# Optimization experiments

Measured on AMD Instinct MI355X. Metric: run time of the kernel, lower is better.

Reference implementation:

```python
import jax, jax.numpy as jnp
import numpy as np

BN_EPS = 1e-5
INTERP_EPS = 1e-8


def setup_inputs() -> dict:
    key = jax.random.key(0)
    ks = jax.random.split(key, 8)
    B, N, S, D1, D2 = 8, 8192, 2048, 128, 256
    C_in, C_mid, C_out = D1 + D2, 256, 256
    return {
        "xyz1": jax.random.normal(ks[0], (B, 3, N), dtype=jnp.float32),
        "xyz2": jax.random.normal(ks[1], (B, 3, S), dtype=jnp.float32),
        "points1": jax.random.normal(ks[2], (B, D1, N), dtype=jnp.float32),
        "points2": jax.random.normal(ks[3], (B, D2, S), dtype=jnp.float32),
        "W0": jax.random.normal(ks[4], (C_mid, C_in), dtype=jnp.float32) * (1.0 / np.sqrt(C_in)),
        "b0": jnp.zeros((C_mid,), dtype=jnp.float32),
        "gamma0": jnp.ones((C_mid,), dtype=jnp.float32),
        "beta0": jnp.zeros((C_mid,), dtype=jnp.float32),
        "W1": jax.random.normal(ks[5], (C_out, C_mid), dtype=jnp.float32) * (1.0 / np.sqrt(C_mid)),
        "b1": jnp.zeros((C_out,), dtype=jnp.float32),
    }


def reference(xyz1, xyz2, points1, points2, W0, b0, gamma0, beta0, W1, b1):
    B, _, N = xyz1.shape
    S = xyz2.shape[2]
    x1 = jnp.transpose(xyz1, (0, 2, 1))  # (B, N, 3)
    x2 = jnpp = jnp.transpose(xyz2, (0, 2, 1))  # (B, S, 3)
    # squared distances: (B, N, S)
    d = (jnp.sum(x1 ** 2, -1)[:, :, None]
         + jnp.sum(x2 ** 2, -1)[:, None, :]
         - 2.0 * jnp.einsum('bnc,bsc->bns', x1, x2))
    # 3 nearest neighbors (fused top-3 instead of full sort; same math)
    neg_d, idx = jax.lax.top_k(-d, 3)  # (B, N, 3)
    dists = -neg_d
    recip = 1.0 / (dists + INTERP_EPS)
    weight = recip / jnp.sum(recip, axis=2, keepdims=True)  # (B, N, 3)
    p2t = jnp.transpose(points2, (0, 2, 1))  # (B, S, D2)
    D2 = p2t.shape[-1]
    gathered = jnp.take_along_axis(p2t, idx.reshape(B, N * 3, 1), axis=1).reshape(B, N, 3, D2)
    interp = jnp.einsum('bnkc,bnk->bcn', gathered, weight)  # (B, D2, N)
    new_points = jnp.concatenate([interp, points1], axis=1)  # (B, D2+D1, N)
    # conv0 (1x1) + BatchNorm (train mode, batch stats) + ReLU
    h = jnp.einsum('oc,bcn->bon', W0, new_points) + b0[None, :, None]
    mean = jnp.mean(h, axis=(0, 2), keepdims=True)
    var = jnp.mean((h - mean) ** 2, axis=(0, 2), keepdims=True)  # biased, as torch BN
    h = gamma0[None, :, None] * (h - mean) * jax.lax.rsqrt(var + BN_EPS) + beta0[None, :, None]
    h = jax.nn.relu(h)
    # conv1 (1x1) + Identity (module pairs conv1 with nn.Identity) + ReLU
    h = jnp.einsum('oc,bcn->bon', W1, h) + b1[None, :, None]
    return jax.nn.relu(h)
```

## Files before the change

kernel.cpp:

```cpp
#include <hip/hip_runtime.h>
#include <stdint.h>

constexpr int B = 8, N = 8192, S = 2048, D1 = 128, D2 = 256;
constexpr int CIN = 384, CMID = 256, COUT = 256;

typedef __attribute__((ext_vector_type(8))) _Float16 half8;
typedef __attribute__((ext_vector_type(4))) _Float16 half4;
typedef __attribute__((ext_vector_type(4))) float f32x4;

union HU { uint32_t u; _Float16 h[2]; };


__global__ __launch_bounds__(256) void k_top3(const float* __restrict__ xyz1,
                                              const float* __restrict__ xyz2,
                                              uint32_t* __restrict__ pw3) {
  __shared__ float4 Pq[S];
  __shared__ float md[4][3][128];
  __shared__ int mi[4][3][128];
  __shared__ float snrm[128];
  const int tid = threadIdx.x;
  const int wv = tid >> 6, lane = tid & 63;
  const int b = blockIdx.y;
  const int nb = blockIdx.x * 128;
  const float* x1 = xyz1 + (size_t)b * 3 * N;
  const float* x2 = xyz2 + (size_t)b * 3 * S;

  for (int j = tid; j < S; j += 256) {
    float sx = x2[j], sy = x2[j + S], sz = x2[j + 2 * S];
    Pq[j] = float4{sx, sy, sz, sx * sx + sy * sy + sz * sz};
  }
  float nax[2], nay[2], naz[2];
#pragma unroll
  for (int t = 0; t < 2; ++t) {
    const int n = nb + t * 64 + lane;
    const float ax = x1[n], ay = x1[n + N], az = x1[n + 2 * N];
    nax[t] = -2.f * ax; nay[t] = -2.f * ay; naz[t] = -2.f * az;
    if (wv == 0) snrm[t * 64 + lane] = ax * ax + ay * ay + az * az;
  }
  __syncthreads();

  float e0[2], e1[2], e2[2];
  int j0[2], j1[2], j2[2];
#pragma unroll
  for (int t = 0; t < 2; ++t) {
    e0[t] = 1e30f; e1[t] = 1e30f; e2[t] = 1e30f;
    j0[t] = 0; j1[t] = 0; j2[t] = 0;
  }
  const int s0 = wv * (S / 4), s1 = s0 + (S / 4);
#pragma unroll 4
  for (int s = s0; s < s1; ++s) {
    const float4 v = Pq[s];
#pragma unroll
    for (int t = 0; t < 2; ++t) {
      const float d = fmaf(nax[t], v.x, fmaf(nay[t], v.y, fmaf(naz[t], v.z, v.w)));
      const bool c0 = d < e0[t], c1 = d < e1[t], c2 = d < e2[t];
      const int u2 = c1 ? j1[t] : s;
      const int u1 = c0 ? j0[t] : s;
      j2[t] = c2 ? u2 : j2[t];
      j1[t] = c1 ? u1 : j1[t];
      j0[t] = c0 ? s : j0[t];
      e2[t] = __builtin_amdgcn_fmed3f(e1[t], e2[t], d);
      e1[t] = __builtin_amdgcn_fmed3f(e0[t], e1[t], d);
      e0[t] = fminf(e0[t], d);
    }
  }
#pragma unroll
  for (int t = 0; t < 2; ++t) {
    const int idx = t * 64 + lane;
    md[wv][0][idx] = e0[t]; mi[wv][0][idx] = j0[t];
    md[wv][1][idx] = e1[t]; mi[wv][1][idx] = j1[t];
    md[wv][2][idx] = e2[t]; mi[wv][2][idx] = j2[t];
  }
  __syncthreads();
  if (tid < 128) {
    float f0 = md[0][0][tid], f1 = md[0][1][tid], f2 = md[0][2][tid];
    int g0 = mi[0][0][tid], g1 = mi[0][1][tid], g2 = mi[0][2][tid];
#pragma unroll
    for (int w = 1; w < 4; ++w)
#pragma unroll
      for (int k = 0; k < 3; ++k) {
        float d = md[w][k][tid];
        int i = mi[w][k][tid];
        if (d < f2) {
          if (d < f1) {
            f2 = f1; g2 = g1;
            if (d < f0) { f1 = f0; g1 = g0; f0 = d; g0 = i; }
            else        { f1 = d;  g1 = i; }
          } else { f2 = d; g2 = i; }
        }
      }
    const float rn = snrm[tid];
    float q0 = fmaxf(f0 + rn, 0.f);
    float q1 = fmaxf(f1 + rn, 0.f);
    float q2 = fmaxf(f2 + rn, 0.f);
    float r0 = 1.0f / (q0 + 1e-8f), r1 = 1.0f / (q1 + 1e-8f), r2 = 1.0f / (q2 + 1e-8f);
    float inv = 1.0f / (r0 + r1 + r2);
    auto pack = [](int i, float w) -> uint32_t {
      uint32_t q = (uint32_t)(w * 2097152.0f + 0.5f);
      if (q > 0x1FFFFFu) q = 0x1FFFFFu;
      return ((uint32_t)i << 21) | q;
    };
    size_t base = ((size_t)b * N + nb + tid) * 3;
    pw3[base]     = pack(g0, r0 * inv);
    pw3[base + 1] = pack(g1, r1 * inv);
    pw3[base + 2] = pack(g2, r2 * inv);
  }
}

__global__ __launch_bounds__(256) void k_G(const float* __restrict__ points2,
                                           const float* __restrict__ W0,
                                           float* __restrict__ dout) {
  __shared__ half8 A_lds[4][256];
  __shared__ half8 B_lds[4][32];
  __shared__ float CT[32][258];
  const int tid = threadIdx.x;
  const int b = blockIdx.x >> 6;
  const int s0 = (blockIdx.x & 63) * 32;
  f32x4 acc[4][2] = {};
  const int wv = tid >> 6, lane = tid & 63;
  const int ln = lane & 15, quad = lane >> 4;
  const int bn = tid & 31, bkc = tid >> 5;
  const int ar = tid >> 3, ac4 = tid & 7;

  for (int kk = 0; kk < 256; kk += 32) {
    __syncthreads();
#pragma unroll
    for (int p = 0; p < 8; ++p) {
      int row = ar + 32 * p;
      const float4 v = *(const float4*)(W0 + (size_t)row * CIN + kk + ac4 * 4);
      half4 hv = {(_Float16)v.x, (_Float16)v.y, (_Float16)v.z, (_Float16)v.w};
      *(half4*)((_Float16*)&A_lds[ac4 >> 1][row] + (ac4 & 1) * 4) = hv;
    }
    {
      half4 hv;
#pragma unroll
      for (int j = 0; j < 4; ++j)
        hv[j] = (_Float16)points2[((size_t)(b * 256 + kk + bkc * 4 + j)) * S + s0 + bn];
      *(half4*)((_Float16*)&B_lds[bkc >> 1][bn] + (bkc & 1) * 4) = hv;
    }
    __syncthreads();
    half8 af[4], bf[2];
#pragma unroll
    for (int i = 0; i < 4; ++i) af[i] = A_lds[quad][wv * 64 + i * 16 + ln];
#pragma unroll
    for (int j = 0; j < 2; ++j) bf[j] = B_lds[quad][j * 16 + ln];
#pragma unroll
    for (int i = 0; i < 4; ++i)
#pragma unroll
      for (int j = 0; j < 2; ++j)
        acc[i][j] = __builtin_amdgcn_mfma_f32_16x16x32_f16(af[i], bf[j], acc[i][j], 0, 0, 0);
  }
  __syncthreads();
#pragma unroll
  for (int i = 0; i < 4; ++i)
#pragma unroll
    for (int reg = 0; reg < 4; ++reg) {
      int row = wv * 64 + i * 16 + quad * 4 + reg;
#pragma unroll
      for (int j = 0; j < 2; ++j) CT[j * 16 + ln][row] = acc[i][j][reg];
    }
  __syncthreads();
  const int sl = tid >> 3, g = tid & 7;
  float* g0 = dout + ((size_t)(b * 256 + 128)) * 8192 + (size_t)(s0 + sl) * 256 + g * 32;
#pragma unroll
  for (int q = 0; q < 8; ++q)
    *(float4*)(g0 + q * 4) = *(const float4*)&CT[sl][g * 32 + q * 4];
}

__global__ __launch_bounds__(256) void k_interp(const uint32_t* __restrict__ pw3,
                                                const float* __restrict__ dout_c,
                                                uint32_t* __restrict__ dout_u) {
  __shared__ int sidx[96];
  __shared__ float sw[96];
  const int tid = threadIdx.x;
  const int b = blockIdx.x >> 8;
  const int n0 = (blockIdx.x & 255) * 32;
  if (tid < 96) {
    uint32_t p = pw3[((size_t)b * N + n0) * 3 + tid];
    sidx[tid] = (int)(p >> 21);
    sw[tid] = (float)(p & 0x1FFFFFu) * (1.0f / 2097152.0f);
  }
  __syncthreads();
  const int colL = tid >> 3, p = tid & 7;
  const float* Gb = dout_c + ((size_t)(b * 256 + 128)) * 8192;
  float a[32];
#pragma unroll
  for (int q = 0; q < 32; ++q) a[q] = 0.f;
#pragma unroll
  for (int k = 0; k < 3; ++k) {
    int j = sidx[colL * 3 + k];
    float w = sw[colL * 3 + k];
    const float* g = Gb + (size_t)j * 256 + p * 32;
#pragma unroll
    for (int q = 0; q < 8; ++q) {
      float4 v = *(const float4*)(g + q * 4);
      a[q * 4 + 0] += w * v.x; a[q * 4 + 1] += w * v.y;
      a[q * 4 + 2] += w * v.z; a[q * 4 + 3] += w * v.w;
    }
  }
#pragma unroll
  for (int q = 0; q < 16; ++q) {
    int cp = p * 16 + q;
    HU u;
    u.h[0] = (_Float16)a[2 * q];
    u.h[1] = (_Float16)a[2 * q + 1];
    dout_u[((size_t)(b * 256 + cp)) * 8192 + n0 + colL] = u.u;
  }
}

__global__ __launch_bounds__(256) void k_w1h(const float* __restrict__ W1,
                                             _Float16* __restrict__ W1h) {
  const int gid = blockIdx.x * 256 + threadIdx.x;
  const float4 v = *(const float4*)(W1 + (size_t)gid * 4);
  half4 h = {(_Float16)v.x, (_Float16)v.y, (_Float16)v.z, (_Float16)v.w};
  *(half4*)(W1h + (size_t)gid * 4) = h;
}

__global__ __launch_bounds__(256) void k_h(uint32_t* __restrict__ h2,
                                           float* __restrict__ dpart,
                                           const float* __restrict__ points1,
                                           const float* __restrict__ W0,
                                           const float* __restrict__ b0) {
  __shared__ half8 A_lds[4][256];
  __shared__ half8 B_lds[4][64];
  __shared__ float red_s[256], red_q[256], sb0[256];
  const int tid = threadIdx.x;
  const int b = blockIdx.x >> 7;
  const int cb = blockIdx.x & 127;
  const int n0 = cb * 64;
  sb0[tid] = b0[tid];
  f32x4 acc[4][4] = {};
  const int wv = tid >> 6, lane = tid & 63;
  const int ln = lane & 15, quad = lane >> 4;
  const int bn = tid & 63, bkc = tid >> 6;
  const int ar = tid >> 3, ac4 = tid & 7;

  for (int kk = 0; kk < 128; kk += 32) {
    __syncthreads();
#pragma unroll
    for (int p = 0; p < 8; ++p) {
      int row = ar + 32 * p;
      const float4 v = *(const float4*)(W0 + (size_t)row * CIN + 256 + kk + ac4 * 4);
      half4 hv = {(_Float16)v.x, (_Float16)v.y, (_Float16)v.z, (_Float16)v.w};
      *(half4*)((_Float16*)&A_lds[ac4 >> 1][row] + (ac4 & 1) * 4) = hv;
    }
    {
      half8 hv;
#pragma unroll
      for (int j = 0; j < 8; ++j)
        hv[j] = (_Float16)points1[((size_t)(b * D1 + kk + bkc * 8 + j)) * N + n0 + bn];
      B_lds[bkc][bn] = hv;
    }
    __syncthreads();
    half8 af[4], bf[4];
#pragma unroll
    for (int i = 0; i < 4; ++i) af[i] = A_lds[quad][wv * 64 + i * 16 + ln];
#pragma unroll
    for (int j = 0; j < 4; ++j) bf[j] = B_lds[quad][j * 16 + ln];
#pragma unroll
    for (int i = 0; i < 4; ++i)
#pragma unroll
      for (int j = 0; j < 4; ++j)
        acc[i][j] = __builtin_amdgcn_mfma_f32_16x16x32_f16(af[i], bf[j], acc[i][j], 0, 0, 0);
  }
#pragma unroll
  for (int i = 0; i < 4; ++i) {
    const int rb = wv * 64 + i * 16 + quad * 4;
    const int cp0 = rb >> 1;
    float rs[4] = {0.f, 0.f, 0.f, 0.f}, rq[4] = {0.f, 0.f, 0.f, 0.f};
#pragma unroll
    for (int jj = 0; jj < 4; ++jj) {
      const int col = n0 + jj * 16 + ln;
      size_t a0 = ((size_t)(b * 256 + cp0)) * 8192 + col;
      HU ua, ub;
      ua.u = h2[a0];
      ub.u = h2[a0 + 8192];
      _Float16 e0 = (_Float16)(acc[i][jj][0] + (float)ua.h[0] + sb0[rb + 0]);
      _Float16 e1 = (_Float16)(acc[i][jj][1] + (float)ua.h[1] + sb0[rb + 1]);
      _Float16 e2 = (_Float16)(acc[i][jj][2] + (float)ub.h[0] + sb0[rb + 2]);
      _Float16 e3 = (_Float16)(acc[i][jj][3] + (float)ub.h[1] + sb0[rb + 3]);
      HU o0, o1;
      o0.h[0] = e0; o0.h[1] = e1; o1.h[0] = e2; o1.h[1] = e3;
      h2[a0] = o0.u;
      h2[a0 + 8192] = o1.u;
      float f0 = (float)e0, f1 = (float)e1, f2 = (float)e2, f3 = (float)e3;
      rs[0] += f0; rq[0] += f0 * f0;
      rs[1] += f1; rq[1] += f1 * f1;
      rs[2] += f2; rq[2] += f2 * f2;
      rs[3] += f3; rq[3] += f3 * f3;
    }
#pragma unroll
    for (int reg = 0; reg < 4; ++reg) {
      float s = rs[reg], q = rq[reg];
#pragma unroll
      for (int m = 1; m < 16; m <<= 1) {
        s += __shfl_xor(s, m);
        q += __shfl_xor(q, m);
      }
      if (ln == 0) { red_s[rb + reg] = s; red_q[rb + reg] = q; }
    }
  }
  __syncthreads();
  float* part = dpart + ((size_t)(b * 256 + 192)) * 8192 + (size_t)cb * 512;
  part[tid] = red_s[tid];
  part[256 + tid] = red_q[tid];
}

__global__ __launch_bounds__(256) void k_bn(const float* __restrict__ dpart,
                                            const float* __restrict__ gamma,
                                            const float* __restrict__ beta,
                                            float* __restrict__ bna,
                                            float* __restrict__ bnb) {
  const int c = blockIdx.x;
  const int tid = threadIdx.x;
  float s = 0.f, q = 0.f;
#pragma unroll
  for (int u = tid; u < 1024; u += 256) {
    int b = u >> 7, cb = u & 127;
    const float* part = dpart + ((size_t)(b * 256 + 192)) * 8192 + (size_t)cb * 512;
    s += part[c];
    q += part[256 + c];
  }
#pragma unroll
  for (int m = 1; m < 64; m <<= 1) {
    s += __shfl_xor(s, m);
    q += __shfl_xor(q, m);
  }
  __shared__ float ls[4], lq[4];
  if ((tid & 63) == 0) { ls[tid >> 6] = s; lq[tid >> 6] = q; }
  __syncthreads();
  if (tid == 0) {
    float st = ls[0] + ls[1] + ls[2] + ls[3];
    float qt = lq[0] + lq[1] + lq[2] + lq[3];
    const float invn = 1.0f / (float)(B * N);
    float mean = st * invn;
    float var = qt * invn - mean * mean;
    float a = gamma[c] * rsqrtf(var + 1e-5f);
    bna[c] = a;
    bnb[c] = beta[c] - mean * a;
  }
}

__global__ __launch_bounds__(256) void k_fused1(const uint32_t* h2,
                                                const _Float16* __restrict__ W1h,
                                                const float* __restrict__ b1,
                                                const float* __restrict__ bna,
                                                const float* __restrict__ bnb,
                                                float* out) {
  __shared__ uint32_t Hh[32 * 33 * 4];
  __shared__ float sa[256], sb[256], sb1[256];
  const int tid = threadIdx.x;
  const int b = blockIdx.x >> 8;
  const int n0 = (blockIdx.x & 255) * 32;
  sa[tid] = bna[tid]; sb[tid] = bnb[tid]; sb1[tid] = b1[tid];
  __syncthreads();
  {
    const int c4 = tid & 7;
    const int rg = tid >> 3;
#pragma unroll
    for (int q = 0; q < 4; ++q) {
      const int cp = rg + 32 * q;
      const uint4 v = *(const uint4*)&h2[((size_t)(b * 256 + cp)) * 8192 + n0 + c4 * 4];
      const int k0 = 2 * cp;
      const float a0 = sa[k0], a1 = sa[k0 + 1], b0v = sb[k0], b1v = sb[k0 + 1];
      const int kc = cp >> 2, sub = cp & 3;
      const uint32_t vv[4] = {v.x, v.y, v.z, v.w};
#pragma unroll
      for (int m = 0; m < 4; ++m) {
        HU u; u.u = vv[m];
        float v0 = a0 * (float)u.h[0] + b0v;
        float v1 = a1 * (float)u.h[1] + b1v;
        HU o;
        o.h[0] = (_Float16)(v0 > 0.f ? v0 : 0.f);
        o.h[1] = (_Float16)(v1 > 0.f ? v1 : 0.f);
        Hh[((kc * 33) + c4 * 4 + m) * 4 + sub] = o.u;
      }
    }
  }
  __syncthreads();
  f32x4 acc[4][2] = {};
  const int wv = tid >> 6, lane = tid & 63;
  const int ln = lane & 15, quad = lane >> 4;
  for (int kk = 0; kk < 256; kk += 32) {
    half8 af[4], bf[2];
#pragma unroll
    for (int i = 0; i < 4; ++i) {
      int row = wv * 64 + i * 16 + ln;
      af[i] = *(const half8*)(W1h + (size_t)row * CMID + kk + quad * 8);
    }
#pragma unroll
    for (int j = 0; j < 2; ++j)
      bf[j] = *(const half8*)&Hh[(((kk >> 3) + quad) * 33 + j * 16 + ln) * 4];
#pragma unroll
    for (int i = 0; i < 4; ++i)
#pragma unroll
      for (int j = 0; j < 2; ++j)
        acc[i][j] = __builtin_amdgcn_mfma_f32_16x16x32_f16(af[i], bf[j], acc[i][j], 0, 0, 0);
  }
#pragma unroll
  for (int i = 0; i < 4; ++i) {
    const int rb = wv * 64 + i * 16 + quad * 4;
#pragma unroll
    for (int reg = 0; reg < 4; ++reg) {
      int row = rb + reg;
      float bias = sb1[row];
      float* orow = out + ((size_t)(b * 256 + row)) * 8192 + n0;
#pragma unroll
      for (int j = 0; j < 2; ++j)
        orow[j * 16 + ln] = fmaxf(acc[i][j][reg] + bias, 0.f);
    }
  }
}

extern "C" void kernel_launch(void* const* d_in, const int* in_sizes, int n_in,
                              void* d_out, int out_size, void* d_ws, size_t ws_size,
                              hipStream_t stream) {
  const float* xyz1 = (const float*)d_in[0];
  const float* xyz2 = (const float*)d_in[1];
  const float* points1 = (const float*)d_in[2];
  const float* points2 = (const float*)d_in[3];
  const float* W0 = (const float*)d_in[4];
  const float* b0 = (const float*)d_in[5];
  const float* gamma0 = (const float*)d_in[6];
  const float* beta0 = (const float*)d_in[7];
  const float* W1 = (const float*)d_in[8];
  const float* b1 = (const float*)d_in[9];
  float* out = (float*)d_out;

  char* ws = (char*)d_ws;
  float* bna = (float*)ws;
  float* bnb = (float*)(ws + 1024);
  uint32_t* pw3 = (uint32_t*)(ws + 2048);
  _Float16* W1h = (_Float16*)(ws + 2048);

  k_top3<<<dim3(N / 128, B), 256, 0, stream>>>(xyz1, xyz2, pw3);
  k_G<<<dim3(B * 64), 256, 0, stream>>>(points2, W0, out);
  k_interp<<<dim3(B * N / 32), 256, 0, stream>>>(pw3, out, (uint32_t*)out);
  k_w1h<<<dim3(64), 256, 0, stream>>>(W1, W1h);
  k_h<<<dim3(B * N / 64), 256, 0, stream>>>((uint32_t*)out, out, points1, W0, b0);
  k_bn<<<dim3(256), 256, 0, stream>>>(out, gamma0, beta0, bna, bnb);
  k_fused1<<<dim3(B * N / 32), 256, 0, stream>>>((const uint32_t*)out, W1h, b1,
                                                 bna, bnb, out);
}
```

Measured before the change: 319.2 us.

## Prepack W0 tail to fp16 and stream A fragments directly in k_h

The fp32-to-fp16 conversion of W0's points1 columns moves into a combined weight-pack kernel, so k_h reads half8 A fragments straight from global memory instead of converting and staging them through LDS every k-step. k_h now uses 32-column tiles (twice as many blocks), loads all of points1 into LDS once with a single barrier, and preloads the interp partial result into the accumulators. It also removes the per-iteration barriers. The cost is more blocks, more BN partials to reduce in k_bn, and repeated global reads of W0h that rely on cache hits.

```diff
diff --git a/kernel.cpp b/kernel.cpp
--- a/kernel.cpp
+++ b/kernel.cpp
@@ -208,59 +208,86 @@
   }
 }
 
-__global__ __launch_bounds__(256) void k_w1h(const float* __restrict__ W1,
-                                             _Float16* __restrict__ W1h) {
-  const int gid = blockIdx.x * 256 + threadIdx.x;
-  const float4 v = *(const float4*)(W1 + (size_t)gid * 4);
-  half4 h = {(_Float16)v.x, (_Float16)v.y, (_Float16)v.z, (_Float16)v.w};
-  *(half4*)(W1h + (size_t)gid * 4) = h;
+__global__ __launch_bounds__(256) void k_wpack(const float* __restrict__ W0,
+                                               const float* __restrict__ W1,
+                                               _Float16* __restrict__ W1h,
+                                               _Float16* __restrict__ W0h) {
+  const int bid = blockIdx.x;
+  if (bid < 64) {
+    const int gid = bid * 256 + threadIdx.x;
+    const float4 v = *(const float4*)(W1 + (size_t)gid * 4);
+    half4 h = {(_Float16)v.x, (_Float16)v.y, (_Float16)v.z, (_Float16)v.w};
+    *(half4*)(W1h + (size_t)gid * 4) = h;
+  } else {
+    const int gid = (bid - 64) * 256 + threadIdx.x;
+    const int row = gid >> 5, c4 = gid & 31;
+    const float4 v = *(const float4*)(W0 + (size_t)row * CIN + 256 + c4 * 4);
+    half4 h = {(_Float16)v.x, (_Float16)v.y, (_Float16)v.z, (_Float16)v.w};
+    *(half4*)(W0h + (size_t)row * 128 + c4 * 4) = h;
+  }
 }
 
 __global__ __launch_bounds__(256) void k_h(uint32_t* __restrict__ h2,
                                            float* __restrict__ dpart,
                                            const float* __restrict__ points1,
-                                           const float* __restrict__ W0,
+                                           const _Float16* __restrict__ W0h,
                                            const float* __restrict__ b0) {
-  __shared__ half8 A_lds[4][256];
-  __shared__ half8 B_lds[4][64];
+  __shared__ half8 B_lds[16][32];
   __shared__ float red_s[256], red_q[256], sb0[256];
   const int tid = threadIdx.x;
-  const int b = blockIdx.x >> 7;
-  const int cb = blockIdx.x & 127;
-  const int n0 = cb * 64;
+  const int b = blockIdx.x >> 8;
+  const int cb = blockIdx.x & 255;
+  const int n0 = cb * 32;
   sb0[tid] = b0[tid];
-  f32x4 acc[4][4] = {};
   const int wv = tid >> 6, lane = tid & 63;
   const int ln = lane & 15, quad = lane >> 4;
-  const int bn = tid & 63, bkc = tid >> 6;
-  const int ar = tid >> 3, ac4 = tid & 7;
-
+
+  f32x4 acc[4][2];
+#pragma unroll
+  for (int i = 0; i < 4; ++i) {
+    const int rb = wv * 64 + i * 16 + quad * 4;
+    const int cp0 = rb >> 1;
+#pragma unroll
+    for (int j = 0; j < 2; ++j) {
+      const int col = n0 + j * 16 + ln;
+      const size_t a0 = ((size_t)(b * 256 + cp0)) * 8192 + col;
+      HU ua, ub;
+      ua.u = h2[a0];
+      ub.u = h2[a0 + 8192];
+      acc[i][j][0] = (float)ua.h[0];
+      acc[i][j][1] = (float)ua.h[1];
+      acc[i][j][2] = (float)ub.h[0];
+      acc[i][j][3] = (float)ub.h[1];
+    }
+  }
+  {
+    const int col = tid & 31;
+    const int kc0 = tid >> 5;
+#pragma unroll
+    for (int it = 0; it < 2; ++it) {
+      const int kc = kc0 + 8 * it;
+      half8 hv;
+#pragma unroll
+      for (int j = 0; j < 8; ++j)
+        hv[j] = (_Float16)points1[((size_t)(b * D1 + kc * 8 + j)) * N + n0 + col];
+      B_lds[kc][col] = hv;
+    }
+  }
+  __syncthreads();
   for (int kk = 0; kk < 128; kk += 32) {
-    __syncthreads();
-#pragma unroll
-    for (int p = 0; p < 8; ++p) {
-      int row = ar + 32 * p;
-      const float4 v = *(const float4*)(W0 + (size_t)row * CIN + 256 + kk + ac4 * 4);
-      half4 hv = {(_Float16)v.x, (_Float16)v.y, (_Float16)v.z, (_Float16)v.w};
-      *(half4*)((_Float16*)&A_lds[ac4 >> 1][row] + (ac4 & 1) * 4) = hv;
-    }
-    {
-      half8 hv;
-#pragma unroll
-      for (int j = 0; j < 8; ++j)
-        hv[j] = (_Float16)points1[((size_t)(b * D1 + kk + bkc * 8 + j)) * N + n0 + bn];
-      B_lds[bkc][bn] = hv;
-    }
-    __syncthreads();
-    half8 af[4], bf[4];
-#pragma unroll
-    for (int i = 0; i < 4; ++i) af[i] = A_lds[quad][wv * 64 + i * 16 + ln];
-#pragma unroll
-    for (int j = 0; j < 4; ++j) bf[j] = B_lds[quad][j * 16 + ln];
+    half8 af[4], bf[2];
+#pragma unroll
+    for (int i = 0; i < 4; ++i) {
+      const int row = wv * 64 + i * 16 + ln;
+      af[i] = *(const half8*)(W0h + (size_t)row * 128 + kk + quad * 8);
+    }
+#pragma unroll
+    for (int j = 0; j < 2; ++j)
+      bf[j] = B_lds[(kk >> 3) + quad][j * 16 + ln];
 #pragma unroll
     for (int i = 0; i < 4; ++i)
 #pragma unroll
-      for (int j = 0; j < 4; ++j)
+      for (int j = 0; j < 2; ++j)
         acc[i][j] = __builtin_amdgcn_mfma_f32_16x16x32_f16(af[i], bf[j], acc[i][j], 0, 0, 0);
   }
 #pragma unroll
@@ -269,16 +296,13 @@
     const int cp0 = rb >> 1;
     float rs[4] = {0.f, 0.f, 0.f, 0.f}, rq[4] = {0.f, 0.f, 0.f, 0.f};
 #pragma unroll
-    for (int jj = 0; jj < 4; ++jj) {
-      const int col = n0 + jj * 16 + ln;
-      size_t a0 = ((size_t)(b * 256 + cp0)) * 8192 + col;
-      HU ua, ub;
-      ua.u = h2[a0];
-      ub.u = h2[a0 + 8192];
-      _Float16 e0 = (_Float16)(acc[i][jj][0] + (float)ua.h[0] + sb0[rb + 0]);
-      _Float16 e1 = (_Float16)(acc[i][jj][1] + (float)ua.h[1] + sb0[rb + 1]);
-      _Float16 e2 = (_Float16)(acc[i][jj][2] + (float)ub.h[0] + sb0[rb + 2]);
-      _Float16 e3 = (_Float16)(acc[i][jj][3] + (float)ub.h[1] + sb0[rb + 3]);
+    for (int j = 0; j < 2; ++j) {
+      const int col = n0 + j * 16 + ln;
+      const size_t a0 = ((size_t)(b * 256 + cp0)) * 8192 + col;
+      _Float16 e0 = (_Float16)(acc[i][j][0] + sb0[rb + 0]);
+      _Float16 e1 = (_Float16)(acc[i][j][1] + sb0[rb + 1]);
+      _Float16 e2 = (_Float16)(acc[i][j][2] + sb0[rb + 2]);
+      _Float16 e3 = (_Float16)(acc[i][j][3] + sb0[rb + 3]);
       HU o0, o1;
       o0.h[0] = e0; o0.h[1] = e1; o1.h[0] = e2; o1.h[1] = e3;
       h2[a0] = o0.u;
@@ -315,8 +339,8 @@
   const int tid = threadIdx.x;
   float s = 0.f, q = 0.f;
 #pragma unroll
-  for (int u = tid; u < 1024; u += 256) {
-    int b = u >> 7, cb = u & 127;
+  for (int u = tid; u < 2048; u += 256) {
+    int b = u >> 8, cb = u & 255;
     const float* part = dpart + ((size_t)(b * 256 + 192)) * 8192 + (size_t)cb * 512;
     s += part[c];
     q += part[256 + c];
@@ -432,12 +456,13 @@
   float* bnb = (float*)(ws + 1024);
   uint32_t* pw3 = (uint32_t*)(ws + 2048);
   _Float16* W1h = (_Float16*)(ws + 2048);
+  _Float16* W0h = (_Float16*)(ws + 2048 + 131072);
 
   k_top3<<<dim3(N / 128, B), 256, 0, stream>>>(xyz1, xyz2, pw3);
   k_G<<<dim3(B * 64), 256, 0, stream>>>(points2, W0, out);
   k_interp<<<dim3(B * N / 32), 256, 0, stream>>>(pw3, out, (uint32_t*)out);
-  k_w1h<<<dim3(64), 256, 0, stream>>>(W1, W1h);
-  k_h<<<dim3(B * N / 64), 256, 0, stream>>>((uint32_t*)out, out, points1, W0, b0);
+  k_wpack<<<dim3(96), 256, 0, stream>>>(W0, W1, W1h, W0h);
+  k_h<<<dim3(B * N / 32), 256, 0, stream>>>((uint32_t*)out, out, points1, W0h, b0);
   k_bn<<<dim3(256), 256, 0, stream>>>(out, gamma0, beta0, bna, bnb);
   k_fused1<<<dim3(B * N / 32), 256, 0, stream>>>((const uint32_t*)out, W1h, b1,
                                                  bna, bnb, out);
```

Result: faster. 309.9 us (-2.9%).
